# Performance work log

Hardware: AMD Instinct MI355X
Metric: run time of the kernel (lower is better)

## Reference

```python
import jax, jax.numpy as jnp
import numpy as np

N_EMBD = 1024
N_HEAD = 16
SEQ = 2048
BATCH = 2
NEG = -1000000000.0


def setup_inputs() -> dict:
    key = jax.random.key(0)
    k0, k1, k2 = jax.random.split(key, 3)
    return {
        "hidden_states": jax.random.normal(k0, (BATCH, SEQ, N_EMBD), dtype=jnp.float32),
        "w_attn": jax.random.normal(k1, (3 * N_EMBD, N_EMBD), dtype=jnp.float32) * 0.02,
        "b_attn": jnp.zeros((3 * N_EMBD,), dtype=jnp.float32),
        "w_proj": jax.random.normal(k2, (N_EMBD, N_EMBD), dtype=jnp.float32) * 0.02,
        "b_proj": jnp.zeros((N_EMBD,), dtype=jnp.float32),
    }


def reference(hidden_states, w_attn, b_attn, w_proj, b_proj):
    B, S, E = hidden_states.shape
    H = N_HEAD
    D = E // H
    # fused qkv projection (Conv1D: x @ kernel.T + bias)
    qkv = hidden_states @ w_attn.T + b_attn  # [B, S, 3E]
    q, k, v = jnp.split(qkv, 3, axis=-1)
    # split heads: [B, S, (H D)] -> [B, H, S, D]
    split = lambda t: t.reshape(B, S, H, D).transpose(0, 2, 1, 3)
    q, k, v = split(q), split(k), split(v)
    # scores [B, H, S, S]
    w = jnp.einsum("bhnd,bhmd->bhnm", q, k) * jax.lax.rsqrt(float(D))
    mask = jnp.tril(jnp.ones((S, S), dtype=jnp.float32))
    w = jnp.where(mask > 0, w, NEG)
    w = jax.nn.softmax(w, axis=-1)
    attn = jnp.einsum("bhnm,bhmd->bhnd", w, v)
    # merge heads -> [B, S, E]
    attn = attn.transpose(0, 2, 1, 3).reshape(B, S, E)
    return attn @ w_proj.T + b_proj
```

## Files before the change

kernel.cpp:

```cpp
#include <hip/hip_runtime.h>
#include <stdint.h>

#define S_LEN  2048
#define EMBD   1024
#define NHEAD  16
#define HDIM   64
#define BATCHN 2
#define ROWS   (BATCHN * S_LEN)

using bf16x8 = __attribute__((ext_vector_type(8))) __bf16;
using f32x4  = __attribute__((ext_vector_type(4))) float;
using f32x16 = __attribute__((ext_vector_type(16))) float;
using u32x4  = __attribute__((ext_vector_type(4))) unsigned;

typedef const __attribute__((address_space(1))) void* gas_ptr;
typedef __attribute__((address_space(3)))       void* las_ptr;

__device__ __forceinline__ void load_lds16(const void* g, void* l) {
    __builtin_amdgcn_global_load_lds((gas_ptr)(uintptr_t)g, (las_ptr)(uintptr_t)l, 16, 0, 0);
}

__device__ __forceinline__ unsigned short f2bf(float f) {
    unsigned u = __builtin_bit_cast(unsigned, f);
    u += 0x7fffu + ((u >> 16) & 1u);
    return (unsigned short)(u >> 16);
}

__device__ __forceinline__ unsigned pkbf(float a, float b) {
    unsigned r;
    asm("v_cvt_pk_bf16_f32 %0, %1, %2" : "=v"(r) : "v"(a), "v"(b));
    return r;
}

__device__ __forceinline__ int swz(int row, int ebase) {
    int byte = (row << 7) + (ebase << 1);
    byte ^= (row & 7) << 4;
    return byte >> 1;
}

__device__ __forceinline__ int swzV(int row, int ebase) {
    int byte = (row << 8) + (ebase << 1);
    byte ^= (row & 15) << 4;
    return byte >> 1;
}

__global__ void cvt3_f32_bf16(const float* __restrict__ s0,
                              const float* __restrict__ s1,
                              const float* __restrict__ s2,
                              unsigned short* __restrict__ d,
                              int n0, int n01, int ntot) {
    int i = blockIdx.x * blockDim.x + threadIdx.x;
    int stride = gridDim.x * blockDim.x;
    for (int idx = i * 4; idx < ntot; idx += stride * 4) {
        const float* s; int off;
        if (idx < n0)       { s = s0; off = idx; }
        else if (idx < n01) { s = s1; off = idx - n0; }
        else                { s = s2; off = idx - n01; }
        float4 f = *(const float4*)(s + off);
        uint2 p;
        p.x = (unsigned)f2bf(f.x) | ((unsigned)f2bf(f.y) << 16);
        p.y = (unsigned)f2bf(f.z) | ((unsigned)f2bf(f.w) << 16);
        *(uint2*)(d + idx) = p;
    }
}

#define SCALE_Q 0.18033688011112042f

template <int MODE>
__global__ __launch_bounds__(256) void gemm_bt(
    const unsigned short* __restrict__ A, const unsigned short* __restrict__ B,
    const float* __restrict__ bias, float* __restrict__ Cout,
    unsigned short* __restrict__ qb, unsigned short* __restrict__ kb,
    unsigned short* __restrict__ vb, int M, int N, int K)
{
    __shared__ __align__(16) unsigned short sA[128 * 64];
    __shared__ __align__(16) unsigned short sB[128 * 64];

    const int tid  = threadIdx.x;
    const int wid  = tid >> 6;
    const int lane = tid & 63;
    const int g    = lane >> 4;
    const int c    = lane & 15;
    const int bm   = blockIdx.x * 128;
    const int bn   = blockIdx.y * 128;
    const int wm   = (wid >> 1) * 64;
    const int wn   = (wid & 1) * 64;

    f32x4 acc[4][4] = {};

    for (int k0 = 0; k0 < K; k0 += 64) {
#pragma unroll
        for (int i = 0; i < 4; ++i) {
            int cidx = i * 256 + tid;
            int row  = cidx >> 3;
            int col  = ((cidx & 7) ^ (row & 7)) << 3;
            load_lds16(A + (size_t)(bm + row) * K + k0 + col,
                       &sA[i * 2048 + wid * 512]);
            load_lds16(B + (size_t)(bn + row) * K + k0 + col,
                       &sB[i * 2048 + wid * 512]);
        }
        __syncthreads();
#pragma unroll
        for (int kk = 0; kk < 2; ++kk) {
            bf16x8 af[4], bfr[4];
#pragma unroll
            for (int i = 0; i < 4; ++i)
                af[i] = *(const bf16x8*)&sA[swz(wm + i * 16 + c, kk * 32 + g * 8)];
#pragma unroll
            for (int j = 0; j < 4; ++j)
                bfr[j] = *(const bf16x8*)&sB[swz(wn + j * 16 + c, kk * 32 + g * 8)];
#pragma unroll
            for (int i = 0; i < 4; ++i)
#pragma unroll
                for (int j = 0; j < 4; ++j)
                    acc[i][j] = __builtin_amdgcn_mfma_f32_16x16x32_bf16(
                        af[i], bfr[j], acc[i][j], 0, 0, 0);
        }
        __syncthreads();
    }

#pragma unroll
    for (int i = 0; i < 4; ++i)
#pragma unroll
        for (int j = 0; j < 4; ++j) {
            int n = bn + wn + j * 16 + c;
            float bv = bias[n];
            if (MODE == 0) {
#pragma unroll
                for (int r = 0; r < 4; ++r) {
                    int m = bm + wm + i * 16 + g * 4 + r;
                    Cout[(size_t)m * N + n] = acc[i][j][r] + bv;
                }
            } else {
                int which = n >> 10, h = (n & 1023) >> 6, d = n & 63;
                if (which < 2) {
                    unsigned short* dst = (which == 0) ? qb : kb;
                    float sc = (which == 0) ? SCALE_Q : 1.0f;
#pragma unroll
                    for (int r = 0; r < 4; ++r) {
                        int m = bm + wm + i * 16 + g * 4 + r;
                        int b = m >> 11, s = m & 2047;
                        dst[(((size_t)b * NHEAD + h) * S_LEN + s) * HDIM + d] =
                            f2bf((acc[i][j][r] + bv) * sc);
                    }
                } else {
                    int m0 = bm + wm + i * 16 + g * 4;
                    int b = m0 >> 11, s0 = m0 & 2047;
                    uint2 p;
                    p.x = pkbf(acc[i][j][0] + bv, acc[i][j][1] + bv);
                    p.y = pkbf(acc[i][j][2] + bv, acc[i][j][3] + bv);
                    *(uint2*)&vb[(((size_t)b * NHEAD + h) * HDIM + d) * S_LEN + s0] = p;
                }
            }
        }
}

__global__ __launch_bounds__(512) void attn_kernel(
    const unsigned short* __restrict__ qbuf, const unsigned short* __restrict__ kbuf,
    const unsigned short* __restrict__ vtbuf, unsigned short* __restrict__ obuf)
{
    __shared__ __align__(16) unsigned short sK[3][128 * 64];
    __shared__ __align__(16) unsigned short sV[3][64 * 128];

    const int tid  = threadIdx.x;
    const int wid  = tid >> 6;
    const int wg   = wid & 3;
    const int grp  = wid >> 2;
    const int lane = tid & 63;
    const int hi   = lane >> 5;
    const int q5   = lane & 31;

    const int x  = blockIdx.x;
    const int j  = x >> 5;
    const int bh = x & 31;
    const int b  = bh >> 4, h = bh & 15;

    const int s  = grp ? j : (15 - j);
    const int TT = 16 - j;

    const unsigned short* Qh = qbuf  + (size_t)bh * S_LEN * HDIM;
    const unsigned short* Kh = kbuf  + (size_t)bh * S_LEN * HDIM;
    const unsigned short* Vt = vtbuf + (size_t)bh * HDIM * S_LEN;

    const int diag64 = 2 * s + (wg >> 1);
    const int qrow0  = 128 * s + 32 * wg;
    const int qg     = qrow0 + q5;

    auto stage = [&](int t, int buf) {
#pragma unroll
        for (int i = 0; i < 4; ++i) {
            int cbase = wg * 256 + i * 64;
            int cidx  = cbase + lane;
            if (grp == 0) {
                int row = cidx >> 3, col = ((cidx & 7) ^ (row & 7)) << 3;
                load_lds16(Kh + (size_t)(t * 128 + row) * HDIM + col,
                           &sK[buf][cbase * 8]);
            } else {
                int row = cidx >> 4, col = ((cidx & 15) ^ (row & 15)) << 3;
                load_lds16(Vt + (size_t)row * S_LEN + t * 128 + col,
                           &sV[buf][cbase * 8]);
            }
        }
    };

    bf16x8 aq[4];
#pragma unroll
    for (int ks = 0; ks < 4; ++ks)
        aq[ks] = *(const bf16x8*)&Qh[(size_t)qg * HDIM + ks * 16 + hi * 8];

    f32x16 o2[2] = {};
    float m_i = -1e30f, l_i = 0.f;

    stage(0, 0);
    stage(1, 1);

    for (int tt = 0; tt < TT; ++tt) {
        const int buf = tt % 3;
        asm volatile("s_waitcnt vmcnt(4)" ::: "memory");
        __builtin_amdgcn_s_barrier();
        stage(tt + 2 < TT ? tt + 2 : TT - 1, (tt + 2) % 3);

#pragma unroll
        for (int half = 0; half < 2; ++half) {
            const int t64 = 2 * tt + half;
            if (t64 > diag64) break;

            f32x16 acc[2] = {};
            __builtin_amdgcn_s_setprio(1);
#pragma unroll
            for (int ks = 0; ks < 4; ++ks) {
                bf16x8 k0 = *(const bf16x8*)&sK[buf][swz(half * 64 + q5,      ks * 16 + hi * 8)];
                bf16x8 k1 = *(const bf16x8*)&sK[buf][swz(half * 64 + q5 + 32, ks * 16 + hi * 8)];
                acc[0] = __builtin_amdgcn_mfma_f32_32x32x16_bf16(k0, aq[ks], acc[0], 0, 0, 0);
                acc[1] = __builtin_amdgcn_mfma_f32_32x32x16_bf16(k1, aq[ks], acc[1], 0, 0, 0);
            }
            __builtin_amdgcn_s_setprio(0);

            if (t64 == diag64) {
#pragma unroll
                for (int t2 = 0; t2 < 2; ++t2) {
                    int base = t64 * 64 + t2 * 32 + 4 * hi;
#pragma unroll
                    for (int r = 0; r < 16; ++r)
                        if (base + (r & 3) + 8 * (r >> 2) > qg) acc[t2][r] = -1e30f;
                }
            }

            float mx[8];
#pragma unroll
            for (int i = 0; i < 8; ++i)
                mx[i] = fmaxf(fmaxf(acc[i >> 2][(i & 3) * 4 + 0], acc[i >> 2][(i & 3) * 4 + 1]),
                              fmaxf(acc[i >> 2][(i & 3) * 4 + 2], acc[i >> 2][(i & 3) * 4 + 3]));
            float pm = fmaxf(fmaxf(fmaxf(mx[0], mx[1]), fmaxf(mx[2], mx[3])),
                             fmaxf(fmaxf(mx[4], mx[5]), fmaxf(mx[6], mx[7])));

            if (__any(pm > m_i + 8.0f)) {
                float pmr   = fmaxf(pm, __shfl_xor(pm, 32, 64));
                float m_new = fmaxf(m_i, pmr);
                float fac, dm = m_i - m_new;
                asm("v_exp_f32 %0, %1" : "=v"(fac) : "v"(dm));
                l_i *= fac;
                m_i  = m_new;
#pragma unroll
                for (int t2 = 0; t2 < 2; ++t2)
#pragma unroll
                    for (int r = 0; r < 16; ++r) o2[t2][r] *= fac;
            }

            unsigned pd[2][8];
            float lsum = 0.f;
#pragma unroll
            for (int t2 = 0; t2 < 2; ++t2) {
                float ev[16];
#pragma unroll
                for (int r = 0; r < 16; ++r) {
                    float a = acc[t2][r] - m_i;
                    asm("v_exp_f32 %0, %1" : "=v"(ev[r]) : "v"(a));
                }
                float s4[4];
#pragma unroll
                for (int u = 0; u < 4; ++u) {
                    s4[u] = (ev[4 * u] + ev[4 * u + 1]) + (ev[4 * u + 2] + ev[4 * u + 3]);
                    pd[t2][2 * u]     = pkbf(ev[4 * u],     ev[4 * u + 1]);
                    pd[t2][2 * u + 1] = pkbf(ev[4 * u + 2], ev[4 * u + 3]);
                }
                lsum += (s4[0] + s4[1]) + (s4[2] + s4[3]);
            }
            l_i += lsum;

            __builtin_amdgcn_s_setprio(1);
#pragma unroll
            for (int ks = 0; ks < 4; ++ks) {
                const int t2 = ks >> 1, k1 = ks & 1;
                unsigned p0 = pd[t2][4 * k1 + 0], p1 = pd[t2][4 * k1 + 1];
                unsigned p2 = pd[t2][4 * k1 + 2], p3 = pd[t2][4 * k1 + 3];
                unsigned s0 = __shfl_xor(p0, 32, 64), s1 = __shfl_xor(p1, 32, 64);
                unsigned s2 = __shfl_xor(p2, 32, 64), s3 = __shfl_xor(p3, 32, 64);
                u32x4 fw;
                fw[0] = hi ? s2 : p0;
                fw[1] = hi ? s3 : p1;
                fw[2] = hi ? p2 : s0;
                fw[3] = hi ? p3 : s1;
                bf16x8 pf = __builtin_bit_cast(bf16x8, fw);
                bf16x8 v0 = *(const bf16x8*)&sV[buf][swzV(q5,      half * 64 + ks * 16 + hi * 8)];
                bf16x8 v1 = *(const bf16x8*)&sV[buf][swzV(q5 + 32, half * 64 + ks * 16 + hi * 8)];
                o2[0] = __builtin_amdgcn_mfma_f32_32x32x16_bf16(v0, pf, o2[0], 0, 0, 0);
                o2[1] = __builtin_amdgcn_mfma_f32_32x32x16_bf16(v1, pf, o2[1], 0, 0, 0);
            }
            __builtin_amdgcn_s_setprio(0);
        }
    }

    asm volatile("s_waitcnt vmcnt(0)" ::: "memory");

    float l_full = l_i + __shfl_xor(l_i, 32, 64);
    float rl = 1.0f / l_full;
    unsigned short* orow = &obuf[((size_t)(b * S_LEN + qg)) * EMBD + h * HDIM];
#pragma unroll
    for (int t2 = 0; t2 < 2; ++t2)
#pragma unroll
        for (int u = 0; u < 4; ++u) {
            uint2 pw;
            pw.x = pkbf(o2[t2][4 * u] * rl,     o2[t2][4 * u + 1] * rl);
            pw.y = pkbf(o2[t2][4 * u + 2] * rl, o2[t2][4 * u + 3] * rl);
            *(uint2*)&orow[t2 * 32 + 4 * hi + 8 * u] = pw;
        }
}

extern "C" void kernel_launch(void* const* d_in, const int* in_sizes, int n_in,
                              void* d_out, int out_size, void* d_ws, size_t ws_size,
                              hipStream_t stream) {
    const float* hidden = (const float*)d_in[0];
    const float* w_attn = (const float*)d_in[1];
    const float* b_attn = (const float*)d_in[2];
    const float* w_proj = (const float*)d_in[3];
    const float* b_proj = (const float*)d_in[4];
    float* out = (float*)d_out;

    unsigned short* Xbf  = (unsigned short*)d_ws;
    unsigned short* Wabf = Xbf  + (size_t)ROWS * EMBD;
    unsigned short* Wpbf = Wabf + (size_t)3 * EMBD * EMBD;
    unsigned short* qb   = Wpbf + (size_t)EMBD * EMBD;
    unsigned short* kb   = qb + (size_t)BATCHN * NHEAD * S_LEN * HDIM;
    unsigned short* vtb  = kb + (size_t)BATCHN * NHEAD * S_LEN * HDIM;
    unsigned short* ob   = vtb + (size_t)BATCHN * NHEAD * S_LEN * HDIM;

    const int n0   = ROWS * EMBD;
    const int n01  = n0 + 3 * EMBD * EMBD;
    const int ntot = n01 + EMBD * EMBD;
    cvt3_f32_bf16<<<2048, 256, 0, stream>>>(hidden, w_attn, w_proj, Xbf,
                                            n0, n01, ntot);

    gemm_bt<1><<<dim3(ROWS / 128, 3 * EMBD / 128), 256, 0, stream>>>(
        Xbf, Wabf, b_attn, nullptr, qb, kb, vtb, ROWS, 3 * EMBD, EMBD);

    attn_kernel<<<dim3(256), 512, 0, stream>>>(qb, kb, vtb, ob);

    gemm_bt<0><<<dim3(ROWS / 128, EMBD / 128), 256, 0, stream>>>(
        ob, Wpbf, b_proj, out, nullptr, nullptr, nullptr, ROWS, EMBD, EMBD);
}
```

Baseline: 112.0 us.

## Add triple-buffered 128x256 QKV GEMM and use permlane32 swap in attention

Replaces the templated GEMM for the QKV projection with a dedicated 512-thread kernel. It uses 128x256 tiles and a three-stage LDS ring fed by async global-to-LDS loads, with waitcnt-based synchronisation and MFMA priority boosts, so loads of later K-tiles overlap compute. The output projection keeps the old single-buffered kernel. In the attention kernel, the lane-32 shuffle-and-select used to build the P operand is replaced with v_permlane32_swap instructions, cutting cross-lane traffic. The larger LDS footprint, 3 x (16 KB + 32 KB), may limit occupancy, and the grid for the QKV GEMM shrinks to 384 blocks.

```diff
diff --git a/kernel.cpp b/kernel.cpp
--- a/kernel.cpp
+++ b/kernel.cpp
@@ -66,12 +66,103 @@
 
 #define SCALE_Q 0.18033688011112042f
 
-template <int MODE>
-__global__ __launch_bounds__(256) void gemm_bt(
+__global__ __launch_bounds__(512, 2) void gemm_qkv(
     const unsigned short* __restrict__ A, const unsigned short* __restrict__ B,
-    const float* __restrict__ bias, float* __restrict__ Cout,
+    const float* __restrict__ bias,
     unsigned short* __restrict__ qb, unsigned short* __restrict__ kb,
-    unsigned short* __restrict__ vb, int M, int N, int K)
+    unsigned short* __restrict__ vb)
+{
+    __shared__ __align__(16) unsigned short sA[3][128 * 64];
+    __shared__ __align__(16) unsigned short sB[3][256 * 64];
+
+    const int tid  = threadIdx.x;
+    const int wid  = tid >> 6;
+    const int lane = tid & 63;
+    const int g    = lane >> 4;
+    const int c    = lane & 15;
+    const int bm   = blockIdx.x * 128;
+    const int bn   = blockIdx.y * 256;
+    const int wm   = (wid >> 2) * 64;
+    const int wn   = (wid & 3) * 64;
+    const int K    = EMBD;
+    const int NKT  = K / 64;
+
+    f32x4 acc[4][4] = {};
+
+    const int r0  = tid >> 3;
+    const int col = ((tid & 7) ^ (r0 & 7)) << 3;
+    auto stage = [&](int kt, int buf) {
+        const int k0 = kt * 64;
+        load_lds16(A + (size_t)(bm + r0) * K + k0 + col,      &sA[buf][wid * 512]);
+        load_lds16(A + (size_t)(bm + 64 + r0) * K + k0 + col, &sA[buf][4096 + wid * 512]);
+#pragma unroll
+        for (int p = 0; p < 4; ++p)
+            load_lds16(B + (size_t)(bn + p * 64 + r0) * K + k0 + col,
+                       &sB[buf][p * 4096 + wid * 512]);
+    };
+
+    stage(0, 0);
+    stage(1, 1);
+
+    for (int kt = 0; kt < NKT; ++kt) {
+        const int buf = kt % 3;
+        asm volatile("s_waitcnt vmcnt(6)" ::: "memory");
+        __builtin_amdgcn_s_barrier();
+        stage(kt + 2 < NKT ? kt + 2 : NKT - 1, (kt + 2) % 3);
+
+#pragma unroll
+        for (int kk = 0; kk < 2; ++kk) {
+            bf16x8 af[4], bfr[4];
+#pragma unroll
+            for (int i = 0; i < 4; ++i)
+                af[i] = *(const bf16x8*)&sA[buf][swz(wm + i * 16 + c, kk * 32 + g * 8)];
+#pragma unroll
+            for (int j = 0; j < 4; ++j)
+                bfr[j] = *(const bf16x8*)&sB[buf][swz(wn + j * 16 + c, kk * 32 + g * 8)];
+            __builtin_amdgcn_s_setprio(1);
+#pragma unroll
+            for (int i = 0; i < 4; ++i)
+#pragma unroll
+                for (int j = 0; j < 4; ++j)
+                    acc[i][j] = __builtin_amdgcn_mfma_f32_16x16x32_bf16(
+                        af[i], bfr[j], acc[i][j], 0, 0, 0);
+            __builtin_amdgcn_s_setprio(0);
+        }
+    }
+
+    asm volatile("s_waitcnt vmcnt(0)" ::: "memory");
+
+#pragma unroll
+    for (int i = 0; i < 4; ++i)
+#pragma unroll
+        for (int j = 0; j < 4; ++j) {
+            int n = bn + wn + j * 16 + c;
+            float bv = bias[n];
+            int which = n >> 10, h = (n & 1023) >> 6, d = n & 63;
+            if (which < 2) {
+                unsigned short* dst = (which == 0) ? qb : kb;
+                float sc = (which == 0) ? SCALE_Q : 1.0f;
+#pragma unroll
+                for (int r = 0; r < 4; ++r) {
+                    int m = bm + wm + i * 16 + g * 4 + r;
+                    int b = m >> 11, s = m & 2047;
+                    dst[(((size_t)b * NHEAD + h) * S_LEN + s) * HDIM + d] =
+                        f2bf((acc[i][j][r] + bv) * sc);
+                }
+            } else {
+                int m0 = bm + wm + i * 16 + g * 4;
+                int b = m0 >> 11, s0 = m0 & 2047;
+                uint2 p;
+                p.x = pkbf(acc[i][j][0] + bv, acc[i][j][1] + bv);
+                p.y = pkbf(acc[i][j][2] + bv, acc[i][j][3] + bv);
+                *(uint2*)&vb[(((size_t)b * NHEAD + h) * HDIM + d) * S_LEN + s0] = p;
+            }
+        }
+}
+
+__global__ __launch_bounds__(256) void gemm_proj(
+    const unsigned short* __restrict__ A, const unsigned short* __restrict__ B,
+    const float* __restrict__ bias, float* __restrict__ Cout, int M, int N, int K)
 {
     __shared__ __align__(16) unsigned short sA[128 * 64];
     __shared__ __align__(16) unsigned short sB[128 * 64];
@@ -125,32 +216,10 @@
         for (int j = 0; j < 4; ++j) {
             int n = bn + wn + j * 16 + c;
             float bv = bias[n];
-            if (MODE == 0) {
-#pragma unroll
-                for (int r = 0; r < 4; ++r) {
-                    int m = bm + wm + i * 16 + g * 4 + r;
-                    Cout[(size_t)m * N + n] = acc[i][j][r] + bv;
-                }
-            } else {
-                int which = n >> 10, h = (n & 1023) >> 6, d = n & 63;
-                if (which < 2) {
-                    unsigned short* dst = (which == 0) ? qb : kb;
-                    float sc = (which == 0) ? SCALE_Q : 1.0f;
-#pragma unroll
-                    for (int r = 0; r < 4; ++r) {
-                        int m = bm + wm + i * 16 + g * 4 + r;
-                        int b = m >> 11, s = m & 2047;
-                        dst[(((size_t)b * NHEAD + h) * S_LEN + s) * HDIM + d] =
-                            f2bf((acc[i][j][r] + bv) * sc);
-                    }
-                } else {
-                    int m0 = bm + wm + i * 16 + g * 4;
-                    int b = m0 >> 11, s0 = m0 & 2047;
-                    uint2 p;
-                    p.x = pkbf(acc[i][j][0] + bv, acc[i][j][1] + bv);
-                    p.y = pkbf(acc[i][j][2] + bv, acc[i][j][3] + bv);
-                    *(uint2*)&vb[(((size_t)b * NHEAD + h) * HDIM + d) * S_LEN + s0] = p;
-                }
+#pragma unroll
+            for (int r = 0; r < 4; ++r) {
+                int m = bm + wm + i * 16 + g * 4 + r;
+                Cout[(size_t)m * N + n] = acc[i][j][r] + bv;
             }
         }
 }
@@ -294,13 +363,10 @@
                 const int t2 = ks >> 1, k1 = ks & 1;
                 unsigned p0 = pd[t2][4 * k1 + 0], p1 = pd[t2][4 * k1 + 1];
                 unsigned p2 = pd[t2][4 * k1 + 2], p3 = pd[t2][4 * k1 + 3];
-                unsigned s0 = __shfl_xor(p0, 32, 64), s1 = __shfl_xor(p1, 32, 64);
-                unsigned s2 = __shfl_xor(p2, 32, 64), s3 = __shfl_xor(p3, 32, 64);
+                asm("v_permlane32_swap_b32 %0, %1" : "+v"(p0), "+v"(p2));
+                asm("v_permlane32_swap_b32 %0, %1" : "+v"(p1), "+v"(p3));
                 u32x4 fw;
-                fw[0] = hi ? s2 : p0;
-                fw[1] = hi ? s3 : p1;
-                fw[2] = hi ? p2 : s0;
-                fw[3] = hi ? p3 : s1;
+                fw[0] = p0; fw[1] = p1; fw[2] = p2; fw[3] = p3;
                 bf16x8 pf = __builtin_bit_cast(bf16x8, fw);
                 bf16x8 v0 = *(const bf16x8*)&sV[buf][swzV(q5,      half * 64 + ks * 16 + hi * 8)];
                 bf16x8 v1 = *(const bf16x8*)&sV[buf][swzV(q5 + 32, half * 64 + ks * 16 + hi * 8)];
@@ -351,11 +417,11 @@
     cvt3_f32_bf16<<<2048, 256, 0, stream>>>(hidden, w_attn, w_proj, Xbf,
                                             n0, n01, ntot);
 
-    gemm_bt<1><<<dim3(ROWS / 128, 3 * EMBD / 128), 256, 0, stream>>>(
-        Xbf, Wabf, b_attn, nullptr, qb, kb, vtb, ROWS, 3 * EMBD, EMBD);
+    gemm_qkv<<<dim3(ROWS / 128, 3 * EMBD / 256), 512, 0, stream>>>(
+        Xbf, Wabf, b_attn, qb, kb, vtb);
 
     attn_kernel<<<dim3(256), 512, 0, stream>>>(qb, kb, vtb, ob);
 
-    gemm_bt<0><<<dim3(ROWS / 128, EMBD / 128), 256, 0, stream>>>(
-        ob, Wpbf, b_proj, out, nullptr, nullptr, nullptr, ROWS, EMBD, EMBD);
-}
+    gemm_proj<<<dim3(ROWS / 128, EMBD / 128), 256, 0, stream>>>(
+        ob, Wpbf, b_proj, out, ROWS, EMBD, EMBD);
+}
```

Result: no change. 112.1 us (+0.0%).
